# Performance work log

Measured on AMD Instinct MI355X. Metric: run time of the kernel, lower is better.

## Reference

```python
import jax, jax.numpy as jnp
import numpy as np

NUM_SECTORS = 11


def setup_inputs() -> dict:
    key = jax.random.key(0)
    k0, k1, k2, k3 = jax.random.split(key, 4)
    B, N, C, H = 4, 2048, 512, 8
    x = jax.random.normal(k0, (B, N, C), dtype=jnp.float32)
    w_qkv = jax.random.normal(k1, (C, 3 * C), dtype=jnp.float32) * 0.02
    w_proj = jax.random.normal(k2, (C, C), dtype=jnp.float32) * 0.02
    b_proj = jnp.zeros((C,), dtype=jnp.float32)
    gate_logit = jnp.full((H,), 2.0, dtype=jnp.float32)
    sector_ids = jax.random.randint(k3, (N,), 0, NUM_SECTORS, dtype=jnp.int64)
    return {"x": x, "w_qkv": w_qkv, "w_proj": w_proj, "b_proj": b_proj,
            "gate_logit": gate_logit, "sector_ids": sector_ids}


def reference(x, w_qkv, w_proj, b_proj, gate_logit, sector_ids):
    B, N, C = x.shape
    H = gate_logit.shape[0]
    d = C // H
    scale = d ** -0.5

    qkv = (x @ w_qkv).reshape(B, N, 3, H, d)
    qkv = jnp.transpose(qkv, (2, 0, 3, 1, 4))  # (3, B, H, N, d)
    q, k, v = qkv[0], qkv[1], qkv[2]

    # Content attention: softmax(QK^T / sqrt(d)) @ V
    attn = jnp.einsum('bhnd,bhmd->bhnm', q, k) * scale
    attn = jax.nn.softmax(attn, axis=-1)
    v_content = jnp.einsum('bhnm,bhmd->bhnd', attn, v)

    # Positional path: A_pos @ V == per-sector mean of V, gathered per row.
    # A_pos[i,j] = 1/|sector(i)| if sector(i)==sector(j); row_sum >= 1 always.
    ids = sector_ids.astype(jnp.int32)
    counts = jax.ops.segment_sum(jnp.ones((N,), x.dtype), ids, num_segments=NUM_SECTORS)
    counts = jnp.maximum(counts, 1.0)
    v_nfirst = jnp.transpose(v, (2, 0, 1, 3)).reshape(N, B * H * d)  # (N, BHd)
    sums = jax.ops.segment_sum(v_nfirst, ids, num_segments=NUM_SECTORS)  # (S, BHd)
    means = sums / counts[:, None]
    v_pos = means[ids].reshape(N, B, H, d).transpose(1, 2, 0, 3)  # (B, H, N, d)

    g = jax.nn.sigmoid(gate_logit)[None, :, None, None]
    out = g * v_pos + (1.0 - g) * v_content  # (B, H, N, d)
    out = jnp.transpose(out, (0, 2, 1, 3)).reshape(B, N, C)
    return out @ w_proj + b_proj
```

## Files before the change

### kernel.cpp

```cpp
#include <hip/hip_runtime.h>
#include <hip/hip_bf16.h>
#include <stdint.h>

typedef float f32x4 __attribute__((ext_vector_type(4)));
typedef float f32x16 __attribute__((ext_vector_type(16)));
typedef short bf16x8 __attribute__((ext_vector_type(8)));
typedef short short4v __attribute__((ext_vector_type(4)));
typedef int i32x4 __attribute__((ext_vector_type(4)));

#define MFMA16(a, b, c) __builtin_amdgcn_mfma_f32_16x16x32_bf16(a, b, c, 0, 0, 0)
#define MFMA32(a, b, c) __builtin_amdgcn_mfma_f32_32x32x16_bf16(a, b, c, 0, 0, 0)

__device__ __forceinline__ float bf2f(unsigned short u) {
    unsigned int x = ((unsigned int)u) << 16;
    float f;
    __builtin_memcpy(&f, &x, 4);
    return f;
}
__device__ __forceinline__ unsigned short f2bf(float f) {
    unsigned int x;
    __builtin_memcpy(&x, &f, 4);
    unsigned int r = x + 0x7FFFu + ((x >> 16) & 1u);
    return (unsigned short)(r >> 16);
}
__device__ __forceinline__ unsigned int cvt_pk_bf16(float lo, float hi) {
    unsigned int d;
    asm("v_cvt_pk_bf16_f32 %0, %1, %2" : "=v"(d) : "v"(lo), "v"(hi));
    return d;
}

#define GLD16(g, l)                                                        \
    __builtin_amdgcn_global_load_lds(                                      \
        (const __attribute__((address_space(1))) void*)(g),                \
        (__attribute__((address_space(3))) void*)(l), 16, 0, 0)

#define QSCALE 0.18033688011112042f

__global__ __launch_bounds__(256) void k_cvt_x(const float* __restrict__ x,
                                               unsigned short* __restrict__ xb) {
    int i = (blockIdx.x * 256 + threadIdx.x) * 4;
    float4 v = *(const float4*)(x + i);
    short4v o;
    o.x = (short)f2bf(v.x);
    o.y = (short)f2bf(v.y);
    o.z = (short)f2bf(v.z);
    o.w = (short)f2bf(v.w);
    *(short4v*)(xb + i) = o;
}

__global__ __launch_bounds__(256) void k_transpose_bf16(const float* __restrict__ in,
                                                        unsigned short* __restrict__ out,
                                                        int R, int C) {
    __shared__ float tile[32][33];
    int tx = threadIdx.x & 31, ty = threadIdx.x >> 5;
    int r0 = blockIdx.y * 32, c0 = blockIdx.x * 32;
#pragma unroll
    for (int i = 0; i < 32; i += 8) tile[ty + i][tx] = in[(r0 + ty + i) * C + c0 + tx];
    __syncthreads();
#pragma unroll
    for (int i = 0; i < 32; i += 8) out[(c0 + ty + i) * R + r0 + tx] = f2bf(tile[tx][ty + i]);
}

__global__ __launch_bounds__(256) void k_gemm_qkv(const unsigned short* __restrict__ A,
                                                  const unsigned short* __restrict__ Bt,
                                                  unsigned short* __restrict__ Q,
                                                  unsigned short* __restrict__ Kd,
                                                  unsigned short* __restrict__ Vr) {
    __shared__ alignas(16) unsigned short As[128 * 64];
    __shared__ alignas(16) unsigned short Bs[128 * 64];
    const int t = threadIdx.x;
    const int w = t >> 6, l = t & 63;
    const int brow = blockIdx.x * 128, bcol = blockIdx.y * 128;
    const int wr = (w >> 1) * 64, wc = (w & 1) * 64;
    const int li = l & 15, lk = (l >> 4) * 8;
    f32x4 acc[4][4] = {};

    for (int kt = 0; kt < 512; kt += 64) {
#pragma unroll
        for (int i = 0; i < 4; i++) {
            int ub = i * 256 + w * 64;
            int r = (ub >> 3) + (l >> 3);
            int ck = l & 7;
            GLD16(A + (brow + r) * 512 + kt + ck * 8, As + ub * 8);
            GLD16(Bt + (bcol + r) * 512 + kt + ck * 8, Bs + ub * 8);
        }
        __syncthreads();
#pragma unroll
        for (int ks = 0; ks < 2; ks++) {
            bf16x8 af[4], bfr[4];
#pragma unroll
            for (int m = 0; m < 4; m++)
                af[m] = *(const bf16x8*)(As + (wr + m * 16 + li) * 64 + ks * 32 + lk);
#pragma unroll
            for (int n = 0; n < 4; n++)
                bfr[n] = *(const bf16x8*)(Bs + (wc + n * 16 + li) * 64 + ks * 32 + lk);
#pragma unroll
            for (int m = 0; m < 4; m++)
#pragma unroll
                for (int n = 0; n < 4; n++)
                    acc[m][n] = MFMA16(af[m], bfr[n], acc[m][n]);
        }
        __syncthreads();
    }
#pragma unroll
    for (int m = 0; m < 4; m++) {
#pragma unroll
        for (int n = 0; n < 4; n++) {
#pragma unroll
            for (int r = 0; r < 4; r++) {
                int gm = brow + wr + m * 16 + (l >> 4) * 4 + r;
                int gn = bcol + wc + n * 16 + li;
                float v = acc[m][n][r];
                int bb = gm >> 11, tok = gm & 2047;
                int three = gn >> 9, hh = (gn >> 6) & 7, dd = gn & 63;
                int bh = bb * 8 + hh;
                if (three == 0)
                    Q[((bh << 11) + tok) * 64 + dd] = f2bf(v * QSCALE);
                else if (three == 1)
                    Kd[((bh << 11) + tok) * 64 + dd] = f2bf(v);
                else
                    Vr[((bh << 11) + tok) * 64 + dd] = f2bf(v);
            }
        }
    }
}

__global__ __launch_bounds__(256) void k_transpose_v(const unsigned short* __restrict__ Vr,
                                                     unsigned short* __restrict__ Vt) {
    __shared__ unsigned short tile[64][68];
    int bh = blockIdx.x >> 5, nt = blockIdx.x & 31;
    int t = threadIdx.x;
    const unsigned short* src = Vr + ((size_t)bh * 2048 + nt * 64) * 64;
#pragma unroll
    for (int i = 0; i < 2; i++) {
        int row = i * 32 + (t >> 3);
        int col = (t & 7) * 8;
        *(bf16x8*)&tile[row][col] = *(const bf16x8*)(src + row * 64 + col);
    }
    __syncthreads();
    unsigned short* dst = Vt + (size_t)bh * 64 * 2048 + nt * 64;
#pragma unroll
    for (int i = 0; i < 2; i++) {
        int drow = i * 32 + (t >> 3);
        int ncol = (t & 7) * 8;
        bf16x8 v;
#pragma unroll
        for (int e = 0; e < 8; e++) v[e] = (short)tile[ncol + e][drow];
        *(bf16x8*)(dst + (size_t)drow * 2048 + ncol) = v;
    }
}

__global__ __launch_bounds__(256, 4) void k_attn(const unsigned short* __restrict__ Q,
                                                 const unsigned short* __restrict__ K,
                                                 const unsigned short* __restrict__ Vt,
                                                 const float* __restrict__ sums,
                                                 const float* __restrict__ invc,
                                                 const int* __restrict__ ids,
                                                 const float* __restrict__ gate,
                                                 unsigned short* __restrict__ mixb) {
    __shared__ alignas(16) unsigned short Ks[2][64 * 64];
    __shared__ alignas(16) unsigned short Vs[2][64 * 64];
    const int bid = blockIdx.x;
    const int bh = bid >> 5, qb = bid & 31;
    const int w = threadIdx.x >> 6, l = threadIdx.x & 63;
    const int wq = w >> 1, wk = w & 1;
    const int q = l & 31, hi = l >> 5;
    const unsigned short* Qh = Q + (size_t)bh * 2048 * 64;
    const char* Kb = (const char*)(K + (size_t)bh * 2048 * 64);
    const char* Vb = (const char*)(Vt + (size_t)bh * 64 * 2048);
    const int qbase = qb * 64 + wq * 32;
    const int swz = (q & 7) << 4;

    bf16x8 qf[4];
#pragma unroll
    for (int ks = 0; ks < 4; ks++)
        qf[ks] = *(const bf16x8*)(Qh + (qbase + q) * 64 + ks * 16 + hi * 8);

    f32x16 o0 = {}, o1 = {};
    float mx = -1e30f, sm = 0.f;

    auto stage = [&](int buf, int kt) {
#pragma unroll
        for (int i = 0; i < 4; i++) {
            int idx = w * 4 + i;
            if (idx < 8) {
                int abase = idx * 1024;
                int al = abase + l * 16;
                int g = al ^ (((al >> 7) & 7) << 4);
                GLD16(Kb + (size_t)kt * 128 + g, (char*)Ks[buf] + abase);
            } else {
                int abase = (idx - 8) * 1024;
                int al = abase + l * 16;
                int row = al >> 7;
                int col = (al & 127) ^ ((row & 7) << 4);
                GLD16(Vb + (size_t)row * 4096 + kt * 2 + col, (char*)Vs[buf] + abase);
            }
        }
    };

    stage(0, 0);
    __syncthreads();

    for (int it = 0; it < 32; ++it) {
        const int cur = it & 1;
        if (it < 31) stage(cur ^ 1, (it + 1) * 64);

        const char* Kc = (const char*)Ks[cur];
        f32x16 s0 = {};
        __builtin_amdgcn_s_setprio(1);
#pragma unroll
        for (int ks = 0; ks < 4; ks++) {
            bf16x8 kf = *(const bf16x8*)(Kc + (wk * 32 + q) * 128 + ((ks * 32 + hi * 16) ^ swz));
            s0 = MFMA32(kf, qf[ks], s0);
        }
        __builtin_amdgcn_s_setprio(0);

        float c8[8];
#pragma unroll
        for (int r = 0; r < 8; r++) c8[r] = fmaxf(s0[r], s0[r + 8]);
#pragma unroll
        for (int r = 0; r < 4; r++) c8[r] = fmaxf(c8[r], c8[r + 4]);
        float tm = fmaxf(fmaxf(c8[0], c8[1]), fmaxf(c8[2], c8[3]));

        if (!__all(tm <= mx + 8.0f)) {
            float tmf = fmaxf(tm, __shfl_xor(tm, 32));
            float mn = fmaxf(mx, tmf);
            float fac = __builtin_amdgcn_exp2f(mx - mn);
            mx = mn;
#pragma unroll
            for (int r = 0; r < 16; r++) {
                o0[r] *= fac;
                o1[r] *= fac;
            }
            sm *= fac;
        }

        float a0 = 0.f, a1 = 0.f, a2 = 0.f, a3 = 0.f;
#pragma unroll
        for (int r = 0; r < 16; r += 4) {
            float p0 = __builtin_amdgcn_exp2f(s0[r] - mx);
            float p1 = __builtin_amdgcn_exp2f(s0[r + 1] - mx);
            float p2 = __builtin_amdgcn_exp2f(s0[r + 2] - mx);
            float p3 = __builtin_amdgcn_exp2f(s0[r + 3] - mx);
            s0[r] = p0;
            s0[r + 1] = p1;
            s0[r + 2] = p2;
            s0[r + 3] = p3;
            a0 += p0;
            a1 += p1;
            a2 += p2;
            a3 += p3;
        }
        sm += (a0 + a1) + (a2 + a3);

        unsigned int pk[4][2];
#pragma unroll
        for (int aa = 0; aa < 4; aa++)
#pragma unroll
            for (int c = 0; c < 2; c++)
                pk[aa][c] = cvt_pk_bf16(s0[4 * aa + 2 * c], s0[4 * aa + 2 * c + 1]);

        const char* Vc = (const char*)Vs[cur];
        __builtin_amdgcn_s_setprio(1);
#pragma unroll
        for (int ksl = 0; ksl < 2; ksl++) {
            unsigned int send0 = hi ? pk[2 * ksl][0] : pk[2 * ksl + 1][0];
            unsigned int send1 = hi ? pk[2 * ksl][1] : pk[2 * ksl + 1][1];
            unsigned int r0 = (unsigned int)__shfl_xor((int)send0, 32);
            unsigned int r1 = (unsigned int)__shfl_xor((int)send1, 32);
            unsigned int u0 = hi ? r0 : pk[2 * ksl][0];
            unsigned int u1 = hi ? r1 : pk[2 * ksl][1];
            unsigned int u2 = hi ? pk[2 * ksl + 1][0] : r0;
            unsigned int u3 = hi ? pk[2 * ksl + 1][1] : r1;
            i32x4 uu = {(int)u0, (int)u1, (int)u2, (int)u3};
            bf16x8 pa = __builtin_bit_cast(bf16x8, uu);
            int vcol = (wk * 64 + ksl * 32 + hi * 16);
            bf16x8 vf0 = *(const bf16x8*)(Vc + q * 128 + (vcol ^ swz));
            bf16x8 vf1 = *(const bf16x8*)(Vc + (q + 32) * 128 + (vcol ^ swz));
            o0 = MFMA32(pa, vf0, o0);
            o1 = MFMA32(pa, vf1, o1);
        }
        __builtin_amdgcn_s_setprio(0);

        __syncthreads();
    }

    sm = sm + __shfl_xor(sm, 32);

    float* So = ((float*)Ks) + wq * 2048;
    float* Sml = ((float*)Vs) + wq * 128;
    if (wk == 1) {
#pragma unroll
        for (int r = 0; r < 16; r++) {
            So[r * 64 + l] = o0[r];
            So[(16 + r) * 64 + l] = o1[r];
        }
        Sml[l] = mx;
        Sml[64 + l] = sm;
    }
    __syncthreads();
    if (wk == 0) {
        float m1 = Sml[l], l1 = Sml[64 + l];
        float ms = fmaxf(mx, m1);
        float f0 = __builtin_amdgcn_exp2f(mx - ms);
        float f1 = __builtin_amdgcn_exp2f(m1 - ms);
        float inv = 1.f / (f0 * sm + f1 * l1);
        float g = 1.f / (1.f + __expf(-gate[bh & 7]));
        float omg = 1.f - g;
        unsigned short* mrow = mixb + (size_t)(bh >> 3) * 2048 * 512 + (bh & 7) * 64;
#pragma unroll
        for (int r = 0; r < 16; r++) {
            float om0 = f0 * o0[r] + f1 * So[r * 64 + l];
            float om1 = f0 * o1[r] + f1 * So[(16 + r) * 64 + l];
            int qq = (r & 3) + 8 * (r >> 2) + 4 * hi;
            float iv = __shfl(inv, qq);
            int tok = qbase + qq;
            int sid = ids[tok];
            float ic = invc[sid];
            float vp0 = sums[((sid * 32 + bh) << 6) + q];
            float vp1 = sums[((sid * 32 + bh) << 6) + q + 32];
            mrow[(size_t)tok * 512 + q] = f2bf(g * vp0 * ic + omg * om0 * iv);
            mrow[(size_t)tok * 512 + q + 32] = f2bf(g * vp1 * ic + omg * om1 * iv);
        }
    }
}

__global__ void k_counts(const int* __restrict__ ids, float* __restrict__ invc) {
    __shared__ float h[11];
    int t = threadIdx.x;
    if (t < 11) h[t] = 0.f;
    __syncthreads();
    for (int n = t; n < 2048; n += 256) atomicAdd(&h[ids[n]], 1.0f);
    __syncthreads();
    if (t < 11) invc[t] = 1.f / fmaxf(h[t], 1.f);
}

__global__ __launch_bounds__(256) void k_sums(const unsigned short* __restrict__ Vt,
                                              const int* __restrict__ ids,
                                              float* __restrict__ sums) {
    __shared__ int ids_s[512];
    int bh = blockIdx.x, ch = blockIdx.y;
    int t = threadIdx.x;
    ids_s[t] = ids[ch * 512 + t];
    ids_s[t + 256] = ids[ch * 512 + 256 + t];
    __syncthreads();
    int dd = t & 63, sub = t >> 6;
    const unsigned short* row = Vt + ((size_t)(bh * 64 + dd) << 11) + ch * 512 + sub * 128;
    const int* idp = ids_s + sub * 128;
    float acc[11] = {};
    for (int i = 0; i < 128; i++) {
        float v = bf2f(row[i]);
        int s = idp[i];
#pragma unroll
        for (int si = 0; si < 11; si++) acc[si] += (s == si) ? v : 0.f;
    }
#pragma unroll
    for (int si = 0; si < 11; si++) atomicAdd(&sums[((si * 32 + bh) << 6) + dd], acc[si]);
}

__global__ __launch_bounds__(256) void k_gemm_out(const unsigned short* __restrict__ A,
                                                  const unsigned short* __restrict__ Bt,
                                                  const float* __restrict__ bias,
                                                  float* __restrict__ out) {
    __shared__ alignas(16) unsigned short As[128 * 64];
    __shared__ alignas(16) unsigned short Bs[128 * 64];
    const int t = threadIdx.x;
    const int w = t >> 6, l = t & 63;
    const int brow = blockIdx.x * 128, bcol = blockIdx.y * 128;
    const int wr = (w >> 1) * 64, wc = (w & 1) * 64;
    const int li = l & 15, lk = (l >> 4) * 8;
    f32x4 acc[4][4] = {};

    for (int kt = 0; kt < 512; kt += 64) {
#pragma unroll
        for (int i = 0; i < 4; i++) {
            int ub = i * 256 + w * 64;
            int r = (ub >> 3) + (l >> 3);
            int ck = l & 7;
            GLD16(A + (brow + r) * 512 + kt + ck * 8, As + ub * 8);
            GLD16(Bt + (bcol + r) * 512 + kt + ck * 8, Bs + ub * 8);
        }
        __syncthreads();
#pragma unroll
        for (int ks = 0; ks < 2; ks++) {
            bf16x8 af[4], bfr[4];
#pragma unroll
            for (int m = 0; m < 4; m++)
                af[m] = *(const bf16x8*)(As + (wr + m * 16 + li) * 64 + ks * 32 + lk);
#pragma unroll
            for (int n = 0; n < 4; n++)
                bfr[n] = *(const bf16x8*)(Bs + (wc + n * 16 + li) * 64 + ks * 32 + lk);
#pragma unroll
            for (int m = 0; m < 4; m++)
#pragma unroll
                for (int n = 0; n < 4; n++)
                    acc[m][n] = MFMA16(af[m], bfr[n], acc[m][n]);
        }
        __syncthreads();
    }
#pragma unroll
    for (int m = 0; m < 4; m++) {
#pragma unroll
        for (int n = 0; n < 4; n++) {
#pragma unroll
            for (int r = 0; r < 4; r++) {
                int gm = brow + wr + m * 16 + (l >> 4) * 4 + r;
                int gn = bcol + wc + n * 16 + li;
                out[(size_t)gm * 512 + gn] = acc[m][n][r] + bias[gn];
            }
        }
    }
}

extern "C" void kernel_launch(void* const* d_in, const int* in_sizes, int n_in,
                              void* d_out, int out_size, void* d_ws, size_t ws_size,
                              hipStream_t stream) {
    const float* x = (const float*)d_in[0];
    const float* w_qkv = (const float*)d_in[1];
    const float* w_proj = (const float*)d_in[2];
    const float* b_proj = (const float*)d_in[3];
    const float* gate = (const float*)d_in[4];
    const int* ids = (const int*)d_in[5];
    float* out = (float*)d_out;
    char* ws = (char*)d_ws;

    unsigned short* xb = (unsigned short*)(ws + 0);
    unsigned short* wqT = (unsigned short*)(ws + 8388608);
    unsigned short* wpT = (unsigned short*)(ws + 9961472);
    unsigned short* Q = (unsigned short*)(ws + 10485760);
    unsigned short* Kd = (unsigned short*)(ws + 18874368);
    unsigned short* Vt = (unsigned short*)(ws + 27262976);
    unsigned short* Vrow = (unsigned short*)(ws + 35651584);
    float* sums = (float*)(ws + 52428800);
    float* invc = (float*)(ws + 52518912);
    unsigned short* mixb = xb;

    hipMemsetAsync(ws + 52428800, 0, 90112 + 64, stream);

    k_cvt_x<<<4096, 256, 0, stream>>>(x, xb);
    {
        dim3 g(48, 16);
        k_transpose_bf16<<<g, 256, 0, stream>>>(w_qkv, wqT, 512, 1536);
    }
    {
        dim3 g(16, 16);
        k_transpose_bf16<<<g, 256, 0, stream>>>(w_proj, wpT, 512, 512);
    }
    {
        dim3 g(64, 12);
        k_gemm_qkv<<<g, 256, 0, stream>>>(xb, wqT, Q, Kd, Vrow);
    }
    k_transpose_v<<<1024, 256, 0, stream>>>(Vrow, Vt);
    k_counts<<<1, 256, 0, stream>>>(ids, invc);
    {
        dim3 g(32, 4);
        k_sums<<<g, 256, 0, stream>>>(Vt, ids, sums);
    }
    k_attn<<<1024, 256, 0, stream>>>(Q, Kd, Vt, sums, invc, ids, gate, mixb);
    {
        dim3 g(64, 4);
        k_gemm_out<<<g, 256, 0, stream>>>(mixb, wpT, b_proj, out);
    }
}
```

Before: 207.3 us.

## Fuse V transpose into QKV GEMM, triple-buffer K in attention, shrink out-GEMM tiles

The QKV GEMM now writes V directly in transposed layout: it stages the tile through a swizzled shared-memory buffer, which removes the separate transpose kernel and the round trip through the Vrow buffer. The attention kernel splits K and V staging, triple-buffers K, and replaces the per-iteration __syncthreads with explicit vmcnt waits plus one barrier, so loads overlap compute more deeply. The output GEMM uses 64x128 tiles to launch twice as many blocks. The costs are more LDS use in attention and hand-written wait counts that must match the number of outstanding loads.

```diff
diff --git a/kernel.cpp b/kernel.cpp
--- a/kernel.cpp
+++ b/kernel.cpp
@@ -65,9 +65,10 @@
                                                   const unsigned short* __restrict__ Bt,
                                                   unsigned short* __restrict__ Q,
                                                   unsigned short* __restrict__ Kd,
-                                                  unsigned short* __restrict__ Vr) {
-    __shared__ alignas(16) unsigned short As[128 * 64];
-    __shared__ alignas(16) unsigned short Bs[128 * 64];
+                                                  unsigned short* __restrict__ Vt) {
+    __shared__ alignas(16) unsigned short smem[128 * 128];
+    unsigned short* As = smem;
+    unsigned short* Bs = smem + 128 * 64;
     const int t = threadIdx.x;
     const int w = t >> 6, l = t & 63;
     const int brow = blockIdx.x * 128, bcol = blockIdx.y * 128;
@@ -102,51 +103,51 @@
         }
         __syncthreads();
     }
-#pragma unroll
-    for (int m = 0; m < 4; m++) {
-#pragma unroll
-        for (int n = 0; n < 4; n++) {
-#pragma unroll
-            for (int r = 0; r < 4; r++) {
-                int gm = brow + wr + m * 16 + (l >> 4) * 4 + r;
-                int gn = bcol + wc + n * 16 + li;
-                float v = acc[m][n][r];
-                int bb = gm >> 11, tok = gm & 2047;
-                int three = gn >> 9, hh = (gn >> 6) & 7, dd = gn & 63;
-                int bh = bb * 8 + hh;
-                if (three == 0)
-                    Q[((bh << 11) + tok) * 64 + dd] = f2bf(v * QSCALE);
-                else if (three == 1)
-                    Kd[((bh << 11) + tok) * 64 + dd] = f2bf(v);
-                else
-                    Vr[((bh << 11) + tok) * 64 + dd] = f2bf(v);
+
+    const int bb = brow >> 11, tok0 = brow & 2047;
+    if (bcol < 1024) {
+#pragma unroll
+        for (int m = 0; m < 4; m++) {
+#pragma unroll
+            for (int n = 0; n < 4; n++) {
+#pragma unroll
+                for (int r = 0; r < 4; r++) {
+                    int gm = brow + wr + m * 16 + (l >> 4) * 4 + r;
+                    int gn = bcol + wc + n * 16 + li;
+                    float v = acc[m][n][r];
+                    int tok = gm & 2047;
+                    int three = gn >> 9, hh = (gn >> 6) & 7, dd = gn & 63;
+                    int bh = bb * 8 + hh;
+                    if (three == 0)
+                        Q[((bh << 11) + tok) * 64 + dd] = f2bf(v * QSCALE);
+                    else
+                        Kd[((bh << 11) + tok) * 64 + dd] = f2bf(v);
+                }
             }
         }
-    }
-}
-
-__global__ __launch_bounds__(256) void k_transpose_v(const unsigned short* __restrict__ Vr,
-                                                     unsigned short* __restrict__ Vt) {
-    __shared__ unsigned short tile[64][68];
-    int bh = blockIdx.x >> 5, nt = blockIdx.x & 31;
-    int t = threadIdx.x;
-    const unsigned short* src = Vr + ((size_t)bh * 2048 + nt * 64) * 64;
-#pragma unroll
-    for (int i = 0; i < 2; i++) {
-        int row = i * 32 + (t >> 3);
-        int col = (t & 7) * 8;
-        *(bf16x8*)&tile[row][col] = *(const bf16x8*)(src + row * 64 + col);
-    }
-    __syncthreads();
-    unsigned short* dst = Vt + (size_t)bh * 64 * 2048 + nt * 64;
-#pragma unroll
-    for (int i = 0; i < 2; i++) {
-        int drow = i * 32 + (t >> 3);
-        int ncol = (t & 7) * 8;
-        bf16x8 v;
-#pragma unroll
-        for (int e = 0; e < 8; e++) v[e] = (short)tile[ncol + e][drow];
-        *(bf16x8*)(dst + (size_t)drow * 2048 + ncol) = v;
+    } else {
+#pragma unroll
+        for (int m = 0; m < 4; m++) {
+#pragma unroll
+            for (int n = 0; n < 4; n++) {
+#pragma unroll
+                for (int r = 0; r < 4; r++) {
+                    int gnl = wc + n * 16 + li;
+                    int gml = wr + m * 16 + (l >> 4) * 4 + r;
+                    smem[gnl * 128 + (gml ^ ((gnl & 7) << 3))] = f2bf(acc[m][n][r]);
+                }
+            }
+        }
+        __syncthreads();
+        int gnl = t >> 1, half = t & 1;
+        int vcol = (bcol - 1024) + gnl;
+        int hh = (vcol >> 6) & 7, dd = vcol & 63;
+        unsigned short* dst = Vt + ((size_t)((bb * 8 + hh) * 64 + dd) << 11) + tok0 + half * 64;
+#pragma unroll
+        for (int j = 0; j < 8; j++) {
+            int elem = (half * 64 + j * 8) ^ ((gnl & 7) << 3);
+            *(bf16x8*)(dst + j * 8) = *(const bf16x8*)&smem[gnl * 128 + elem];
+        }
     }
 }
 
@@ -158,7 +159,7 @@
                                                  const int* __restrict__ ids,
                                                  const float* __restrict__ gate,
                                                  unsigned short* __restrict__ mixb) {
-    __shared__ alignas(16) unsigned short Ks[2][64 * 64];
+    __shared__ alignas(16) unsigned short Ks[3][64 * 64];
     __shared__ alignas(16) unsigned short Vs[2][64 * 64];
     const int bid = blockIdx.x;
     const int bh = bid >> 5, qb = bid & 31;
@@ -179,33 +180,45 @@
     f32x16 o0 = {}, o1 = {};
     float mx = -1e30f, sm = 0.f;
 
-    auto stage = [&](int buf, int kt) {
-#pragma unroll
-        for (int i = 0; i < 4; i++) {
-            int idx = w * 4 + i;
-            if (idx < 8) {
-                int abase = idx * 1024;
-                int al = abase + l * 16;
-                int g = al ^ (((al >> 7) & 7) << 4);
-                GLD16(Kb + (size_t)kt * 128 + g, (char*)Ks[buf] + abase);
-            } else {
-                int abase = (idx - 8) * 1024;
-                int al = abase + l * 16;
-                int row = al >> 7;
-                int col = (al & 127) ^ ((row & 7) << 4);
-                GLD16(Vb + (size_t)row * 4096 + kt * 2 + col, (char*)Vs[buf] + abase);
-            }
+    auto stageK = [&](int buf, int kt) {
+#pragma unroll
+        for (int i = 0; i < 2; i++) {
+            int abase = (w * 2 + i) * 1024;
+            int al = abase + l * 16;
+            int g = al ^ (((al >> 7) & 7) << 4);
+            GLD16(Kb + (size_t)kt * 128 + g, (char*)Ks[buf] + abase);
         }
     };
-
-    stage(0, 0);
-    __syncthreads();
-
+    auto stageV = [&](int buf, int kt) {
+#pragma unroll
+        for (int i = 0; i < 2; i++) {
+            int abase = (w * 2 + i) * 1024;
+            int al = abase + l * 16;
+            int row = al >> 7;
+            int col = (al & 127) ^ ((row & 7) << 4);
+            GLD16(Vb + (size_t)row * 4096 + kt * 2 + col, (char*)Vs[buf] + abase);
+        }
+    };
+
+    stageK(0, 0);
+    stageV(0, 0);
+    stageK(1, 64);
+
+#pragma unroll 1
     for (int it = 0; it < 32; ++it) {
-        const int cur = it & 1;
-        if (it < 31) stage(cur ^ 1, (it + 1) * 64);
-
-        const char* Kc = (const char*)Ks[cur];
+        if (it < 31)
+            asm volatile("s_waitcnt vmcnt(2)" ::: "memory");
+        else
+            asm volatile("s_waitcnt vmcnt(0)" ::: "memory");
+        __builtin_amdgcn_sched_barrier(0);
+        __builtin_amdgcn_s_barrier();
+        __builtin_amdgcn_sched_barrier(0);
+
+        if (it < 31) stageV((it + 1) & 1, (it + 1) * 64);
+        __builtin_amdgcn_sched_barrier(0);
+        if (it < 30) stageK((it + 2) % 3, (it + 2) * 64);
+
+        const char* Kc = (const char*)Ks[it % 3];
         f32x16 s0 = {};
         __builtin_amdgcn_s_setprio(1);
 #pragma unroll
@@ -260,7 +273,7 @@
             for (int c = 0; c < 2; c++)
                 pk[aa][c] = cvt_pk_bf16(s0[4 * aa + 2 * c], s0[4 * aa + 2 * c + 1]);
 
-        const char* Vc = (const char*)Vs[cur];
+        const char* Vc = (const char*)Vs[it & 1];
         __builtin_amdgcn_s_setprio(1);
 #pragma unroll
         for (int ksl = 0; ksl < 2; ksl++) {
@@ -281,9 +294,9 @@
             o1 = MFMA32(pa, vf1, o1);
         }
         __builtin_amdgcn_s_setprio(0);
-
-        __syncthreads();
-    }
+    }
+
+    __syncthreads();
 
     sm = sm + __shfl_xor(sm, 32);
 
@@ -362,38 +375,44 @@
                                                   const unsigned short* __restrict__ Bt,
                                                   const float* __restrict__ bias,
                                                   float* __restrict__ out) {
-    __shared__ alignas(16) unsigned short As[128 * 64];
+    __shared__ alignas(16) unsigned short As[64 * 64];
     __shared__ alignas(16) unsigned short Bs[128 * 64];
     const int t = threadIdx.x;
     const int w = t >> 6, l = t & 63;
-    const int brow = blockIdx.x * 128, bcol = blockIdx.y * 128;
-    const int wr = (w >> 1) * 64, wc = (w & 1) * 64;
+    const int brow = blockIdx.x * 64, bcol = blockIdx.y * 128;
+    const int wc = w * 32;
     const int li = l & 15, lk = (l >> 4) * 8;
-    f32x4 acc[4][4] = {};
+    f32x4 acc[4][2] = {};
 
     for (int kt = 0; kt < 512; kt += 64) {
+#pragma unroll
+        for (int i = 0; i < 2; i++) {
+            int ub = i * 256 + w * 64;
+            int r = (ub >> 3) + (l >> 3);
+            int ck = l & 7;
+            GLD16(A + (brow + r) * 512 + kt + ck * 8, As + ub * 8);
+        }
 #pragma unroll
         for (int i = 0; i < 4; i++) {
             int ub = i * 256 + w * 64;
             int r = (ub >> 3) + (l >> 3);
             int ck = l & 7;
-            GLD16(A + (brow + r) * 512 + kt + ck * 8, As + ub * 8);
             GLD16(Bt + (bcol + r) * 512 + kt + ck * 8, Bs + ub * 8);
         }
         __syncthreads();
 #pragma unroll
         for (int ks = 0; ks < 2; ks++) {
-            bf16x8 af[4], bfr[4];
+            bf16x8 af[4], bfr[2];
 #pragma unroll
             for (int m = 0; m < 4; m++)
-                af[m] = *(const bf16x8*)(As + (wr + m * 16 + li) * 64 + ks * 32 + lk);
-#pragma unroll
-            for (int n = 0; n < 4; n++)
+                af[m] = *(const bf16x8*)(As + (m * 16 + li) * 64 + ks * 32 + lk);
+#pragma unroll
+            for (int n = 0; n < 2; n++)
                 bfr[n] = *(const bf16x8*)(Bs + (wc + n * 16 + li) * 64 + ks * 32 + lk);
 #pragma unroll
             for (int m = 0; m < 4; m++)
 #pragma unroll
-                for (int n = 0; n < 4; n++)
+                for (int n = 0; n < 2; n++)
                     acc[m][n] = MFMA16(af[m], bfr[n], acc[m][n]);
         }
         __syncthreads();
@@ -401,10 +420,10 @@
 #pragma unroll
     for (int m = 0; m < 4; m++) {
 #pragma unroll
-        for (int n = 0; n < 4; n++) {
+        for (int n = 0; n < 2; n++) {
 #pragma unroll
             for (int r = 0; r < 4; r++) {
-                int gm = brow + wr + m * 16 + (l >> 4) * 4 + r;
+                int gm = brow + m * 16 + (l >> 4) * 4 + r;
                 int gn = bcol + wc + n * 16 + li;
                 out[(size_t)gm * 512 + gn] = acc[m][n][r] + bias[gn];
             }
@@ -430,7 +449,6 @@
     unsigned short* Q = (unsigned short*)(ws + 10485760);
     unsigned short* Kd = (unsigned short*)(ws + 18874368);
     unsigned short* Vt = (unsigned short*)(ws + 27262976);
-    unsigned short* Vrow = (unsigned short*)(ws + 35651584);
     float* sums = (float*)(ws + 52428800);
     float* invc = (float*)(ws + 52518912);
     unsigned short* mixb = xb;
@@ -448,9 +466,8 @@
     }
     {
         dim3 g(64, 12);
-        k_gemm_qkv<<<g, 256, 0, stream>>>(xb, wqT, Q, Kd, Vrow);
-    }
-    k_transpose_v<<<1024, 256, 0, stream>>>(Vrow, Vt);
+        k_gemm_qkv<<<g, 256, 0, stream>>>(xb, wqT, Q, Kd, Vt);
+    }
     k_counts<<<1, 256, 0, stream>>>(ids, invc);
     {
         dim3 g(32, 4);
@@ -458,7 +475,7 @@
     }
     k_attn<<<1024, 256, 0, stream>>>(Q, Kd, Vt, sums, invc, ids, gate, mixb);
     {
-        dim3 g(64, 4);
+        dim3 g(128, 4);
         k_gemm_out<<<g, 256, 0, stream>>>(mixb, wpT, b_proj, out);
     }
 }
```

Measured after the change: 199.7 us. 1.04x faster.
